# Performance work log

Hardware: AMD Instinct MI355X
Metric: run time of the kernel (lower is better)

The kernel has to match this reference:

```python
import jax, jax.numpy as jnp
import numpy as np

D_MODEL = 1024
N_HEADS = 16
D_K = D_MODEL // N_HEADS


def setup_inputs() -> dict:
    key = jax.random.key(0)
    ks = jax.random.split(key, 9)
    B, L = 2, 2048
    s = 1.0 / np.sqrt(D_MODEL)
    return {
        "x": jax.random.normal(ks[0], (B, L, D_MODEL), dtype=jnp.float32),
        "Wq": jax.random.normal(ks[1], (D_MODEL, D_MODEL), dtype=jnp.float32) * s,
        "bq": jnp.zeros((D_MODEL,), dtype=jnp.float32),
        "Wk": jax.random.normal(ks[2], (D_MODEL, D_MODEL), dtype=jnp.float32) * s,
        "bk": jnp.zeros((D_MODEL,), dtype=jnp.float32),
        "Wv": jax.random.normal(ks[3], (D_MODEL, D_MODEL), dtype=jnp.float32) * s,
        "bv": jnp.zeros((D_MODEL,), dtype=jnp.float32),
        "Wo": jax.random.normal(ks[4], (D_MODEL, D_MODEL), dtype=jnp.float32) * s,
        "bo": jnp.zeros((D_MODEL,), dtype=jnp.float32),
    }


def reference(x, Wq, bq, Wk, bk, Wv, bv, Wo, bo):
    B, L, D = x.shape
    H, dk = N_HEADS, D_K
    # torch Linear: y = x @ W.T + b
    def proj(W, b):
        y = jnp.einsum('bld,ed->ble', x, W) + b
        return y.reshape(B, L, H, dk).transpose(0, 2, 1, 3)  # [B,H,L,dk]
    Q = proj(Wq, bq)
    K = proj(Wk, bk)
    V = proj(Wv, bv)
    scores = jnp.einsum('bhqd,bhkd->bhqk', Q, K) / jnp.sqrt(jnp.float32(dk))
    probs = jax.nn.softmax(scores, axis=-1)
    # intervention: zero column 0, then average with original -> halve column 0
    col_scale = jnp.where(jnp.arange(L) == 0, 0.5, 1.0).astype(probs.dtype)
    combined = probs * col_scale  # broadcast over last axis
    out = jnp.einsum('bhqk,bhkd->bhqd', combined, V)
    out = out.transpose(0, 2, 1, 3).reshape(B, L, D)
    # dropout in eval mode = identity
    return jnp.einsum('bld,ed->ble', out, Wo) + bo
```

## Files before the change

### kernel.cpp

```cpp
#include <hip/hip_runtime.h>
#include <stdint.h>

#define DMODEL 1024
#define LSEQ   2048
#define NBATCH 2
#define NHEADS 16
#define DKH    64
#define MROWS  4096

typedef __attribute__((ext_vector_type(8))) short short8;
typedef __attribute__((ext_vector_type(4))) float f32x4;
typedef __attribute__((ext_vector_type(16))) float f32x16;
typedef __attribute__((ext_vector_type(2))) int int2v;

__device__ __forceinline__ unsigned short f2b(float f) {
  union { float f; unsigned int u; } v; v.f = f;
  unsigned int r = v.u + 0x7FFFu + ((v.u >> 16) & 1u);
  return (unsigned short)(r >> 16);
}

__device__ __forceinline__ float b2f(unsigned short u) {
  union { unsigned int i; float f; } v; v.i = ((unsigned int)u) << 16; return v.f;
}

__device__ __forceinline__ unsigned int cvtpk(float lo, float hi) {
  unsigned int r;
  asm volatile("v_cvt_pk_bf16_f32 %0, %1, %2" : "=v"(r) : "v"(lo), "v"(hi));
  return r;
}

__device__ __forceinline__ int2v pl32swap(unsigned int a, unsigned int b) {
  return __builtin_amdgcn_permlane32_swap((int)a, (int)b, false, false);
}

__device__ __forceinline__ void async16(const void* g, void* l) {
  __builtin_amdgcn_global_load_lds(
      (const __attribute__((address_space(1))) unsigned int*)g,
      (__attribute__((address_space(3))) unsigned int*)l, 16, 0, 0);
}

__global__ void k_cvtall(const float* __restrict__ x,
                         const float* __restrict__ w0, const float* __restrict__ w1,
                         const float* __restrict__ w2, const float* __restrict__ w3,
                         unsigned short* __restrict__ xb,
                         unsigned short* __restrict__ d0, unsigned short* __restrict__ d1,
                         unsigned short* __restrict__ d2, unsigned short* __restrict__ d3) {
  const int y = blockIdx.y;
  const float* s; unsigned short* d;
  switch (y) {
    case 0: case 1: case 2: case 3:
      s = x + (size_t)y * 1048576; d = xb + (size_t)y * 1048576; break;
    case 4: s = w0; d = d0; break;
    case 5: s = w1; d = d1; break;
    case 6: s = w2; d = d2; break;
    default: s = w3; d = d3; break;
  }
  const int i = blockIdx.x * blockDim.x + threadIdx.x;
  float4 v = ((const float4*)s)[i];
  ushort4 o;
  o.x = f2b(v.x); o.y = f2b(v.y); o.z = f2b(v.z); o.w = f2b(v.w);
  ((ushort4*)d)[i] = o;
}

__device__ __forceinline__ void gemm_mainloop(
    const unsigned short* __restrict__ A, const unsigned short* __restrict__ B,
    int rowBase, int colBase, char* As, char* Bs, f32x4 acc[4][4])
{
  const int tid  = threadIdx.x;
  const int lane = tid & 63;
  const int wr   = tid >> 7;
  const int wc   = (tid >> 6) & 1;
  for (int kt = 0; kt < DMODEL / 64; ++kt) {
    const int k0 = kt * 64;
    __syncthreads();
#pragma unroll
    for (int p = 0; p < 4; ++p) {
      const int chunk = p * 256 + tid;
      const int row   = chunk >> 3;
      const int cs    = (chunk & 7) ^ (row & 7);
      async16(A + (size_t)(rowBase + row) * DMODEL + k0 + cs * 8,
              As + (p * 256 + (tid & 0xC0)) * 16);
      async16(B + (size_t)(colBase + row) * DMODEL + k0 + cs * 8,
              Bs + (p * 256 + (tid & 0xC0)) * 16);
    }
    __syncthreads();
#pragma unroll
    for (int ks = 0; ks < 2; ++ks) {
      short8 af[4], bfr[4];
#pragma unroll
      for (int m = 0; m < 4; ++m) {
        const int ra = wr * 64 + m * 16 + (lane & 15);
        af[m]  = *(const short8*)(As + ra * 128 + (((ks * 4 + (lane >> 4)) ^ (ra & 7)) * 16));
        const int rb = wc * 64 + m * 16 + (lane & 15);
        bfr[m] = *(const short8*)(Bs + rb * 128 + (((ks * 4 + (lane >> 4)) ^ (rb & 7)) * 16));
      }
#pragma unroll
      for (int m = 0; m < 4; ++m)
#pragma unroll
        for (int n = 0; n < 4; ++n)
          acc[m][n] = __builtin_amdgcn_mfma_f32_16x16x32_bf16(af[m], bfr[n], acc[m][n], 0, 0, 0);
    }
  }
}

__global__ __launch_bounds__(256, 2) void k_gemm_qkv(
    const unsigned short* __restrict__ xb,
    const unsigned short* __restrict__ Wqb, const unsigned short* __restrict__ Wkb,
    const unsigned short* __restrict__ Wvb,
    const float* __restrict__ bq, const float* __restrict__ bk, const float* __restrict__ bv,
    unsigned short* __restrict__ Q, unsigned short* __restrict__ Ksw,
    unsigned short* __restrict__ Vsw)
{
  __shared__ char As[16384];
  __shared__ char Bs[16384];
  const int z = blockIdx.z;
  const unsigned short* W = (z == 0) ? Wqb : ((z == 1) ? Wkb : Wvb);
  const float* bias       = (z == 0) ? bq  : ((z == 1) ? bk  : bv);
  const int rowBase = blockIdx.x * 128, colBase = blockIdx.y * 128;

  f32x4 zero = {0.f, 0.f, 0.f, 0.f};
  f32x4 acc[4][4];
#pragma unroll
  for (int m = 0; m < 4; ++m)
#pragma unroll
    for (int n = 0; n < 4; ++n) acc[m][n] = zero;

  gemm_mainloop(xb, W, rowBase, colBase, As, Bs, acc);

  const int tid = threadIdx.x, lane = tid & 63;
  const int wr = tid >> 7, wc = (tid >> 6) & 1;
  const float scale = (z == 0) ? 0.18033688011112042f : 1.0f;
#pragma unroll
  for (int m = 0; m < 4; ++m) {
#pragma unroll
    for (int n = 0; n < 4; ++n) {
      const int gcol = colBase + wc * 64 + n * 16 + (lane & 15);
      const float bb = bias[gcol];
      const int h = gcol >> 6, d = gcol & 63;
      if (z == 0) {
#pragma unroll
        for (int r = 0; r < 4; ++r) {
          const int grow = rowBase + wr * 64 + m * 16 + ((lane >> 4) << 2) + r;
          const int bi = grow >> 11, l = grow & 2047;
          Q[(((size_t)(bi * NHEADS + h)) * LSEQ + l) * DKH + d] =
              f2b((acc[m][n][r] + bb) * scale);
        }
      } else if (z == 1) {
#pragma unroll
        for (int r = 0; r < 4; ++r) {
          const int grow = rowBase + wr * 64 + m * 16 + ((lane >> 4) << 2) + r;
          const int bi = grow >> 11, l = grow & 2047;
          const int bh = bi * NHEADS + h;
          Ksw[(size_t)(bh * 32 + (l >> 6)) * 4096 + ((d >> 3) * 64 + (l & 63)) * 8 + (d & 7)] =
              f2b(acc[m][n][r] + bb);
        }
      } else {
        const int grow0 = rowBase + wr * 64 + m * 16 + ((lane >> 4) << 2);
        const int bi = grow0 >> 11, l0 = grow0 & 2047;
        const int bh = bi * NHEADS + h;
        ushort4 o;
        o.x = f2b(acc[m][n][0] + bb);
        o.y = f2b(acc[m][n][1] + bb);
        o.z = f2b(acc[m][n][2] + bb);
        o.w = f2b(acc[m][n][3] + bb);
        *(ushort4*)(Vsw + (size_t)(bh * 32 + (l0 >> 6)) * 4096 +
                    (((l0 & 63) >> 3) * 64 + d) * 8 + (l0 & 7)) = o;
      }
    }
  }
}

template <int NSPLIT>
__global__ __launch_bounds__(256, 4) void k_attn(
    const unsigned short* __restrict__ Q, const unsigned short* __restrict__ Ksw,
    const unsigned short* __restrict__ Vsw,
    unsigned short* __restrict__ O0, unsigned short* __restrict__ O1,
    unsigned short* __restrict__ O2, unsigned short* __restrict__ O3,
    float* __restrict__ Lp)
{
  __shared__ char Ks[2][8192];
  __shared__ char Vs[2][8192];

  const int tid = threadIdx.x, lane = tid & 63, w = tid >> 6;
  const int hi = lane >> 5;
  const int ql = lane & 31;

  const int GROUPS = 32 * NSPLIT;
  const int flat = blockIdx.x;
  const int g  = flat & (GROUPS - 1);
  const int qi = flat / GROUPS;
  const int bh = g / NSPLIT, ks = g & (NSPLIT - 1);
  const int b = bh >> 4, h = bh & 15;
  const int q0 = qi * 128 + w * 32;

  unsigned short* __restrict__ Op =
      (ks == 0) ? O0 : ((ks == 1) ? O1 : ((ks == 2) ? O2 : O3));
  const unsigned short* __restrict__ Qh = Q + (size_t)bh * LSEQ * DKH;

  short8 qf[4];
#pragma unroll
  for (int c = 0; c < 4; ++c)
    qf[c] = *(const short8*)(Qh + (size_t)(q0 + ql) * DKH + c * 16 + hi * 8);

  union { unsigned short u[8]; short8 v; } ones;
#pragma unroll
  for (int j = 0; j < 8; ++j) ones.u[j] = 0x3F80;

  f32x16 oacc[2], lacc, z16;
#pragma unroll
  for (int r = 0; r < 16; ++r) {
    oacc[0][r] = 0.f; oacc[1][r] = 0.f; lacc[r] = 0.f; z16[r] = 0.f;
  }
  float p0 = 0.f;

  auto stage = [&](int buf, int kt2) {
    const unsigned short* Kt = Ksw + (size_t)(bh * 32 + kt2) * 4096;
    const unsigned short* Vt = Vsw + (size_t)(bh * 32 + kt2) * 4096;
#pragma unroll
    for (int p = 0; p < 2; ++p) {
      const int c = p * 256 + tid;
      async16(Kt + c * 8, Ks[buf] + (p * 256 + (tid & 0xC0)) * 16);
      async16(Vt + c * 8, Vs[buf] + (p * 256 + (tid & 0xC0)) * 16);
    }
  };

  const int NT = 32 / NSPLIT;
  const int t0 = ks * NT;

  stage(0, t0);
  __syncthreads();

  int cur = 0;
  for (int it = 0; it < NT; ++it) {
    if (it < NT - 1) stage(cur ^ 1, t0 + it + 1);
    const char* Kc = Ks[cur];
    const char* Vc = Vs[cur];

    f32x16 sv[2];
#pragma unroll
    for (int b2 = 0; b2 < 2; ++b2) {
      short8 kf = *(const short8*)(Kc + ((0 * 2 + hi) * 64 + b2 * 32 + ql) * 16);
      sv[b2] = __builtin_amdgcn_mfma_f32_32x32x16_bf16(kf, qf[0], z16, 0, 0, 0);
    }
#pragma unroll
    for (int c = 1; c < 4; ++c) {
#pragma unroll
      for (int b2 = 0; b2 < 2; ++b2) {
        short8 kf = *(const short8*)(Kc + ((c * 2 + hi) * 64 + b2 * 32 + ql) * 16);
        sv[b2] = __builtin_amdgcn_mfma_f32_32x32x16_bf16(kf, qf[c], sv[b2], 0, 0, 0);
      }
    }

#pragma unroll
    for (int b2 = 0; b2 < 2; ++b2)
#pragma unroll
      for (int r = 0; r < 16; ++r) sv[b2][r] = __builtin_amdgcn_exp2f(sv[b2][r]);

    if (ks == 0 && it == 0 && hi == 0) { p0 = sv[0][0]; sv[0][0] *= 0.5f; }

    unsigned int pk[2][4][2];
#pragma unroll
    for (int b2 = 0; b2 < 2; ++b2)
#pragma unroll
      for (int R = 0; R < 4; ++R) {
        pk[b2][R][0] = cvtpk(sv[b2][4 * R + 0], sv[b2][4 * R + 1]);
        pk[b2][R][1] = cvtpk(sv[b2][4 * R + 2], sv[b2][4 * R + 3]);
      }

#pragma unroll
    for (int kc = 0; kc < 4; ++kc) {
      const int b2 = kc >> 1, Rl = 2 * (kc & 1);
      int2v sw0 = pl32swap(pk[b2][Rl][0], pk[b2][Rl + 1][0]);
      int2v sw1 = pl32swap(pk[b2][Rl][1], pk[b2][Rl + 1][1]);
      union { int i[4]; short8 v; } pa;
      pa.i[0] = sw0[0]; pa.i[1] = sw1[0]; pa.i[2] = sw0[1]; pa.i[3] = sw1[1];
      lacc = __builtin_amdgcn_mfma_f32_32x32x16_bf16(pa.v, ones.v, lacc, 0, 0, 0);
#pragma unroll
      for (int n = 0; n < 2; ++n) {
        short8 vb = *(const short8*)(Vc + ((kc * 2 + hi) * 64 + n * 32 + ql) * 16);
        oacc[n] = __builtin_amdgcn_mfma_f32_32x32x16_bf16(pa.v, vb, oacc[n], 0, 0, 0);
      }
    }

    __syncthreads();
    cur ^= 1;
  }

#pragma unroll
  for (int r = 0; r < 16; ++r) {
    const int qrow = (r & 3) + 8 * (r >> 2) + 4 * hi;
    float lv = lacc[r];
    if (ks == 0) lv += 0.5f * __shfl(p0, qrow);
#pragma unroll
    for (int n = 0; n < 2; ++n) {
      Op[(size_t)(b * LSEQ + q0 + qrow) * DMODEL + h * 64 + n * 32 + ql] =
          f2b(oacc[n][r]);
    }
    if (ql == 0)
      Lp[ks * (32 * LSEQ) + bh * LSEQ + q0 + qrow] = lv;
  }
}

template <int NSPLIT>
__global__ void k_combine(const unsigned short* __restrict__ o0,
                          const unsigned short* __restrict__ o1,
                          const unsigned short* __restrict__ o2,
                          const unsigned short* __restrict__ o3,
                          const float* __restrict__ Lp,
                          unsigned short* __restrict__ AO)
{
  const int i = blockIdx.x * blockDim.x + threadIdx.x;
  const int row = i >> 7;
  const int q = row & 2047, b = row >> 11;
  const int h = (i & 127) >> 3;
  const int bhq = (b * 16 + h) * 2048 + q;
  float ltot = Lp[bhq] + Lp[32 * LSEQ + bhq];
  if (NSPLIT == 4) ltot += Lp[2 * 32 * LSEQ + bhq] + Lp[3 * 32 * LSEQ + bhq];
  const float inv = 1.0f / ltot;
  short8 a = ((const short8*)o0)[i];
  short8 c = ((const short8*)o1)[i];
  union { unsigned short u[8]; short8 v; } o;
  if (NSPLIT == 2) {
#pragma unroll
    for (int j = 0; j < 8; ++j)
      o.u[j] = f2b((b2f((unsigned short)a[j]) + b2f((unsigned short)c[j])) * inv);
  } else {
    short8 d = ((const short8*)o2)[i];
    short8 e = ((const short8*)o3)[i];
#pragma unroll
    for (int j = 0; j < 8; ++j)
      o.u[j] = f2b((b2f((unsigned short)a[j]) + b2f((unsigned short)c[j]) +
                    b2f((unsigned short)d[j]) + b2f((unsigned short)e[j])) * inv);
  }
  ((short8*)AO)[i] = o.v;
}

__global__ __launch_bounds__(256, 2) void k_gemm_out(
    const unsigned short* __restrict__ AO, const unsigned short* __restrict__ Wob,
    const float* __restrict__ bo, float* __restrict__ out)
{
  __shared__ char As[16384];
  __shared__ char Bs[16384];
  const int rowBase = blockIdx.x * 128, colBase = blockIdx.y * 128;
  f32x4 zero = {0.f, 0.f, 0.f, 0.f};
  f32x4 acc[4][4];
#pragma unroll
  for (int m = 0; m < 4; ++m)
#pragma unroll
    for (int n = 0; n < 4; ++n) acc[m][n] = zero;

  gemm_mainloop(AO, Wob, rowBase, colBase, As, Bs, acc);

  const int tid = threadIdx.x, lane = tid & 63;
  const int wr = tid >> 7, wc = (tid >> 6) & 1;
#pragma unroll
  for (int m = 0; m < 4; ++m) {
#pragma unroll
    for (int n = 0; n < 4; ++n) {
      const int gcol = colBase + wc * 64 + n * 16 + (lane & 15);
      const float bb = bo[gcol];
#pragma unroll
      for (int r = 0; r < 4; ++r) {
        const int grow = rowBase + wr * 64 + m * 16 + ((lane >> 4) << 2) + r;
        out[(size_t)grow * DMODEL + gcol] = acc[m][n][r] + bb;
      }
    }
  }
}

extern "C" void kernel_launch(void* const* d_in, const int* in_sizes, int n_in,
                              void* d_out, int out_size, void* d_ws, size_t ws_size,
                              hipStream_t stream) {
  const float* x  = (const float*)d_in[0];
  const float* Wq = (const float*)d_in[1];
  const float* bq = (const float*)d_in[2];
  const float* Wk = (const float*)d_in[3];
  const float* bk = (const float*)d_in[4];
  const float* Wv = (const float*)d_in[5];
  const float* bv = (const float*)d_in[6];
  const float* Wo = (const float*)d_in[7];
  const float* bo = (const float*)d_in[8];
  float* out = (float*)d_out;
  char* ws = (char*)d_ws;

  const size_t MB = 1u << 20;
  unsigned short* xb  = (unsigned short*)(ws);
  unsigned short* Wob = (unsigned short*)(ws + 8  * MB);
  float*          Lpp = (float*)(ws + 10 * MB);
  unsigned short* Wqb = (unsigned short*)(ws + 10 * MB);
  unsigned short* Wkb = (unsigned short*)(ws + 12 * MB);
  unsigned short* Wvb = (unsigned short*)(ws + 14 * MB);
  unsigned short* Qb  = (unsigned short*)(ws + 16 * MB);
  unsigned short* AOb = (unsigned short*)(ws + 16 * MB);
  unsigned short* Ksw = (unsigned short*)(ws + 24 * MB);
  unsigned short* Vsw = (unsigned short*)(ws + 32 * MB);
  unsigned short* Op0 = (unsigned short*)(ws);
  unsigned short* Op1 = (unsigned short*)(ws + 40 * MB);
  unsigned short* Op2 = (unsigned short*)(ws + 48 * MB);
  unsigned short* Op3 = (unsigned short*)(ws + 56 * MB);


  dim3 gcv(1024, 8);
  k_cvtall<<<gcv, 256, 0, stream>>>(x, Wq, Wk, Wv, Wo, xb, Wqb, Wkb, Wvb, Wob);

  dim3 gqkv(MROWS / 128, DMODEL / 128, 3);
  k_gemm_qkv<<<gqkv, 256, 0, stream>>>(xb, Wqb, Wkb, Wvb, bq, bk, bv, Qb, Ksw, Vsw);

  const bool big = ws_size >= 64 * MB;
  if (big) {
    k_attn<4><<<16 * 32 * 4, 256, 0, stream>>>(Qb, Ksw, Vsw, Op0, Op1, Op2, Op3, Lpp);
    k_combine<4><<<2048, 256, 0, stream>>>(Op0, Op1, Op2, Op3, Lpp, AOb);
  } else {
    k_attn<2><<<16 * 32 * 2, 256, 0, stream>>>(Qb, Ksw, Vsw, Op0, Op1, Op1, Op1, Lpp);
    k_combine<2><<<2048, 256, 0, stream>>>(Op0, Op1, Op1, Op1, Lpp, AOb);
  }

  dim3 gout(MROWS / 128, DMODEL / 128);
  k_gemm_out<<<gout, 256, 0, stream>>>(AOb, Wob, bo, out);
}
```

Measured before the change: 121.4 us.

## Drop split-K attention and combine kernel; normalize in attention epilogue

Removes the key-dimension split of the attention kernel and the separate combine kernel. Each block now walks all 32 key tiles for its query block and divides by the row sum before writing bf16 output straight into the attention-output buffer. This removes the partial-output and row-sum traffic plus one kernel launch. In exchange the grid shrinks from 2048 (or 1024) blocks to 512, which lowers parallelism on a GPU with many CUs and makes each block's loop longer.

```diff
diff --git a/kernel.cpp b/kernel.cpp
--- a/kernel.cpp
+++ b/kernel.cpp
@@ -170,13 +170,10 @@
   }
 }
 
-template <int NSPLIT>
 __global__ __launch_bounds__(256, 4) void k_attn(
     const unsigned short* __restrict__ Q, const unsigned short* __restrict__ Ksw,
     const unsigned short* __restrict__ Vsw,
-    unsigned short* __restrict__ O0, unsigned short* __restrict__ O1,
-    unsigned short* __restrict__ O2, unsigned short* __restrict__ O3,
-    float* __restrict__ Lp)
+    unsigned short* __restrict__ AO)
 {
   __shared__ char Ks[2][8192];
   __shared__ char Vs[2][8192];
@@ -185,16 +182,12 @@
   const int hi = lane >> 5;
   const int ql = lane & 31;
 
-  const int GROUPS = 32 * NSPLIT;
   const int flat = blockIdx.x;
-  const int g  = flat & (GROUPS - 1);
-  const int qi = flat / GROUPS;
-  const int bh = g / NSPLIT, ks = g & (NSPLIT - 1);
+  const int bh = flat & 31;
+  const int qi = flat >> 5;
   const int b = bh >> 4, h = bh & 15;
   const int q0 = qi * 128 + w * 32;
 
-  unsigned short* __restrict__ Op =
-      (ks == 0) ? O0 : ((ks == 1) ? O1 : ((ks == 2) ? O2 : O3));
   const unsigned short* __restrict__ Qh = Q + (size_t)bh * LSEQ * DKH;
 
   short8 qf[4];
@@ -224,15 +217,14 @@
     }
   };
 
-  const int NT = 32 / NSPLIT;
-  const int t0 = ks * NT;
-
-  stage(0, t0);
+  const int NT = 32;
+
+  stage(0, 0);
   __syncthreads();
 
   int cur = 0;
   for (int it = 0; it < NT; ++it) {
-    if (it < NT - 1) stage(cur ^ 1, t0 + it + 1);
+    if (it < NT - 1) stage(cur ^ 1, it + 1);
     const char* Kc = Ks[cur];
     const char* Vc = Vs[cur];
 
@@ -256,7 +248,7 @@
 #pragma unroll
       for (int r = 0; r < 16; ++r) sv[b2][r] = __builtin_amdgcn_exp2f(sv[b2][r]);
 
-    if (ks == 0 && it == 0 && hi == 0) { p0 = sv[0][0]; sv[0][0] *= 0.5f; }
+    if (it == 0 && hi == 0) { p0 = sv[0][0]; sv[0][0] *= 0.5f; }
 
     unsigned int pk[2][4][2];
 #pragma unroll
@@ -289,50 +281,14 @@
 #pragma unroll
   for (int r = 0; r < 16; ++r) {
     const int qrow = (r & 3) + 8 * (r >> 2) + 4 * hi;
-    float lv = lacc[r];
-    if (ks == 0) lv += 0.5f * __shfl(p0, qrow);
+    const float lv = lacc[r] + 0.5f * __shfl(p0, qrow);
+    const float inv = 1.0f / lv;
 #pragma unroll
     for (int n = 0; n < 2; ++n) {
-      Op[(size_t)(b * LSEQ + q0 + qrow) * DMODEL + h * 64 + n * 32 + ql] =
-          f2b(oacc[n][r]);
-    }
-    if (ql == 0)
-      Lp[ks * (32 * LSEQ) + bh * LSEQ + q0 + qrow] = lv;
-  }
-}
-
-template <int NSPLIT>
-__global__ void k_combine(const unsigned short* __restrict__ o0,
-                          const unsigned short* __restrict__ o1,
-                          const unsigned short* __restrict__ o2,
-                          const unsigned short* __restrict__ o3,
-                          const float* __restrict__ Lp,
-                          unsigned short* __restrict__ AO)
-{
-  const int i = blockIdx.x * blockDim.x + threadIdx.x;
-  const int row = i >> 7;
-  const int q = row & 2047, b = row >> 11;
-  const int h = (i & 127) >> 3;
-  const int bhq = (b * 16 + h) * 2048 + q;
-  float ltot = Lp[bhq] + Lp[32 * LSEQ + bhq];
-  if (NSPLIT == 4) ltot += Lp[2 * 32 * LSEQ + bhq] + Lp[3 * 32 * LSEQ + bhq];
-  const float inv = 1.0f / ltot;
-  short8 a = ((const short8*)o0)[i];
-  short8 c = ((const short8*)o1)[i];
-  union { unsigned short u[8]; short8 v; } o;
-  if (NSPLIT == 2) {
-#pragma unroll
-    for (int j = 0; j < 8; ++j)
-      o.u[j] = f2b((b2f((unsigned short)a[j]) + b2f((unsigned short)c[j])) * inv);
-  } else {
-    short8 d = ((const short8*)o2)[i];
-    short8 e = ((const short8*)o3)[i];
-#pragma unroll
-    for (int j = 0; j < 8; ++j)
-      o.u[j] = f2b((b2f((unsigned short)a[j]) + b2f((unsigned short)c[j]) +
-                    b2f((unsigned short)d[j]) + b2f((unsigned short)e[j])) * inv);
-  }
-  ((short8*)AO)[i] = o.v;
+      AO[(size_t)(b * LSEQ + q0 + qrow) * DMODEL + h * 64 + n * 32 + ql] =
+          f2b(oacc[n][r] * inv);
+    }
+  }
 }
 
 __global__ __launch_bounds__(256, 2) void k_gemm_out(
@@ -385,20 +341,14 @@
 
   const size_t MB = 1u << 20;
   unsigned short* xb  = (unsigned short*)(ws);
+  unsigned short* AOb = (unsigned short*)(ws);
   unsigned short* Wob = (unsigned short*)(ws + 8  * MB);
-  float*          Lpp = (float*)(ws + 10 * MB);
   unsigned short* Wqb = (unsigned short*)(ws + 10 * MB);
   unsigned short* Wkb = (unsigned short*)(ws + 12 * MB);
   unsigned short* Wvb = (unsigned short*)(ws + 14 * MB);
   unsigned short* Qb  = (unsigned short*)(ws + 16 * MB);
-  unsigned short* AOb = (unsigned short*)(ws + 16 * MB);
   unsigned short* Ksw = (unsigned short*)(ws + 24 * MB);
   unsigned short* Vsw = (unsigned short*)(ws + 32 * MB);
-  unsigned short* Op0 = (unsigned short*)(ws);
-  unsigned short* Op1 = (unsigned short*)(ws + 40 * MB);
-  unsigned short* Op2 = (unsigned short*)(ws + 48 * MB);
-  unsigned short* Op3 = (unsigned short*)(ws + 56 * MB);
-
 
   dim3 gcv(1024, 8);
   k_cvtall<<<gcv, 256, 0, stream>>>(x, Wq, Wk, Wv, Wo, xb, Wqb, Wkb, Wvb, Wob);
@@ -406,14 +356,7 @@
   dim3 gqkv(MROWS / 128, DMODEL / 128, 3);
   k_gemm_qkv<<<gqkv, 256, 0, stream>>>(xb, Wqb, Wkb, Wvb, bq, bk, bv, Qb, Ksw, Vsw);
 
-  const bool big = ws_size >= 64 * MB;
-  if (big) {
-    k_attn<4><<<16 * 32 * 4, 256, 0, stream>>>(Qb, Ksw, Vsw, Op0, Op1, Op2, Op3, Lpp);
-    k_combine<4><<<2048, 256, 0, stream>>>(Op0, Op1, Op2, Op3, Lpp, AOb);
-  } else {
-    k_attn<2><<<16 * 32 * 2, 256, 0, stream>>>(Qb, Ksw, Vsw, Op0, Op1, Op1, Op1, Lpp);
-    k_combine<2><<<2048, 256, 0, stream>>>(Op0, Op1, Op1, Op1, Lpp, AOb);
-  }
+  k_attn<<<16 * 32, 256, 0, stream>>>(Qb, Ksw, Vsw, AOb);
 
   dim3 gout(MROWS / 128, DMODEL / 128);
   k_gemm_out<<<gout, 256, 0, stream>>>(AOb, Wob, bo, out);
```

Measured after the change: 109.8 us. 1.11x faster.
